# Performance work log

Measured on AMD Instinct MI355X. Metric: run time of the kernel, lower is better.

Reference implementation:

```python
import jax, jax.numpy as jnp
import numpy as np

B, T, D = 2, 2048, 2048
H, HKV, HD = 16, 8, 128
R = 128            # virtual memory tokens
DFF = 6144
MAX_ALPHA = 0.5
INFERENCE_SCALE = 1.0
EPS = 1e-6
NEG = -1e9


def _rms_norm(x, w):
    return x * jax.lax.rsqrt(jnp.mean(x * x, axis=-1, keepdims=True) + EPS) * w


def _rotate_half(x):
    x1, x2 = jnp.split(x, 2, axis=-1)
    return jnp.concatenate([-x2, x1], axis=-1)


def setup_inputs() -> dict:
    key = jax.random.key(0)
    ks = jax.random.split(key, 16)
    s = 0.02  # weight init scale
    hidden_states = jax.random.normal(ks[0], (B, T, D), jnp.float32)
    key_extra = jax.random.normal(ks[1], (B, HKV, R, HD), jnp.float32)
    value_extra = jax.random.normal(ks[2], (B, HKV, R, HD), jnp.float32)
    # RoPE tables (rope_theta = 1e6 as in Qwen3)
    inv_freq = 1.0 / (1e6 ** (jnp.arange(0, HD, 2, dtype=jnp.float32) / HD))
    freqs = jnp.arange(T, dtype=jnp.float32)[:, None] * inv_freq[None, :]  # (T, HD/2)
    emb = jnp.concatenate([freqs, freqs], axis=-1)  # (T, HD)
    cos, sin = jnp.cos(emb), jnp.sin(emb)
    # additive causal mask (B,1,T,T)
    causal = jnp.tril(jnp.ones((T, T), dtype=bool))
    attention_mask = jnp.where(causal, 0.0, NEG).astype(jnp.float32)
    attention_mask = jnp.broadcast_to(attention_mask[None, None], (B, 1, T, T))
    init_alpha, max_alpha = 0.1, MAX_ALPHA
    alpha_logit = jnp.float32(np.log(init_alpha / (max_alpha - init_alpha + 1e-8)))
    return {
        "hidden_states": hidden_states,
        "key_extra": key_extra,
        "value_extra": value_extra,
        "cos": cos,
        "sin": sin,
        "attention_mask": attention_mask,
        "alpha_logit": alpha_logit,
        "Wq": jax.random.normal(ks[3], (D, H * HD), jnp.float32) * s,
        "Wk": jax.random.normal(ks[4], (D, HKV * HD), jnp.float32) * s,
        "Wv": jax.random.normal(ks[5], (D, HKV * HD), jnp.float32) * s,
        "Wo": jax.random.normal(ks[6], (H * HD, D), jnp.float32) * s,
        "q_norm_w": jnp.ones((HD,), jnp.float32),
        "k_norm_w": jnp.ones((HD,), jnp.float32),
        "ln1_w": jnp.ones((D,), jnp.float32),
        "ln2_w": jnp.ones((D,), jnp.float32),
        "Wg": jax.random.normal(ks[7], (D, DFF), jnp.float32) * s,
        "Wu": jax.random.normal(ks[8], (D, DFF), jnp.float32) * s,
        "Wd": jax.random.normal(ks[9], (DFF, D), jnp.float32) * s,
    }


def reference(hidden_states, key_extra, value_extra, cos, sin, attention_mask,
              alpha_logit, Wq, Wk, Wv, Wo, q_norm_w, k_norm_w, ln1_w, ln2_w,
              Wg, Wu, Wd):
    Bq, Tq, Dq = hidden_states.shape
    G = H // HKV  # num_key_value_groups
    scaling = HD ** -0.5

    # ---- alpha scaling of raw memory KV (RawKVInjector.get_alpha) ----
    alpha = MAX_ALPHA * jax.nn.sigmoid(alpha_logit)
    eff = alpha * INFERENCE_SCALE
    k_extra = key_extra * eff
    v_extra = value_extra * eff

    # ---- decoder layer: input_layernorm ----
    residual = hidden_states
    h = _rms_norm(hidden_states, ln1_w)

    # ---- QKV projections + per-head RMSNorm ----
    q = _rms_norm((h @ Wq).reshape(Bq, Tq, H, HD), q_norm_w).transpose(0, 2, 1, 3)    # (B,H,T,hd)
    k = _rms_norm((h @ Wk).reshape(Bq, Tq, HKV, HD), k_norm_w).transpose(0, 2, 1, 3)  # (B,Hkv,T,hd)
    v = (h @ Wv).reshape(Bq, Tq, HKV, HD).transpose(0, 2, 1, 3)                        # (B,Hkv,T,hd)

    # ---- RoPE (applied before virtual-KV concat; virtual tokens get no RoPE) ----
    c, s_ = cos[None, None], sin[None, None]  # (1,1,T,hd)
    q = q * c + _rotate_half(q) * s_
    k = k * c + _rotate_half(k) * s_

    # ---- prepend virtual memory KV ----
    k_all = jnp.concatenate([k_extra, k], axis=2)  # (B,Hkv,R+T,hd)
    v_all = jnp.concatenate([v_extra, v], axis=2)
    Tk = R + Tq

    # mask: virtual tokens fully visible (zeros), then causal
    virtual_mask = jnp.zeros((Bq, 1, Tq, R), attention_mask.dtype)
    mask_full = jnp.concatenate([virtual_mask, attention_mask], axis=-1)  # (B,1,T,R+T)

    # ---- GQA attention (grouped einsum == repeat_kv + matmul) ----
    qg = q.reshape(Bq, HKV, G, Tq, HD)
    scores = jnp.einsum('bkgth,bksh->bkgts', qg, k_all) * scaling  # (B,Hkv,G,T,Tk)
    scores = scores + mask_full[:, :, None]
    probs = jax.nn.softmax(scores.astype(jnp.float32), axis=-1).astype(q.dtype)
    attn = jnp.einsum('bkgts,bksh->bkgth', probs, v_all)           # (B,Hkv,G,T,hd)
    attn = attn.reshape(Bq, H, Tq, HD).transpose(0, 2, 1, 3).reshape(Bq, Tq, H * HD)
    attn = attn @ Wo

    hidden = residual + attn

    # ---- MLP (SwiGLU) ----
    residual = hidden
    h2 = _rms_norm(hidden, ln2_w)
    mlp = (jax.nn.silu(h2 @ Wg) * (h2 @ Wu)) @ Wd
    return residual + mlp
```

## Files before the change

kernel.cpp:

```cpp
#include <hip/hip_runtime.h>
#include <hip/hip_bf16.h>


#define DEV __device__ __forceinline__

using f32x4  = __attribute__((ext_vector_type(4))) float;
using bf16x8 = __attribute__((ext_vector_type(8))) short;

constexpr int B_ = 2, T_ = 2048, D_ = 2048, H_ = 16, HKV_ = 8, HD_ = 128;
constexpr int R_ = 128, DFF_ = 6144, TK_ = R_ + T_;
constexpr int NT64_ = TK_ / 64;
constexpr int QKVW_ = 4096;
constexpr float EPS_ = 1e-6f;
constexpr float SCALING_ = 0.08838834764831845f;

DEV float bf2f(unsigned short u) {
  unsigned int x = ((unsigned int)u) << 16;
  return __builtin_bit_cast(float, x);
}
DEV unsigned short f2bf(float f) {
  unsigned int x = __builtin_bit_cast(unsigned int, f);
  x += 0x7fffu + ((x >> 16) & 1u);
  return (unsigned short)(x >> 16);
}

DEV void gload_lds16(const void* g, void* l) {
  __builtin_amdgcn_global_load_lds((__attribute__((address_space(1))) void*)(g),
                                   (__attribute__((address_space(3))) void*)(l),
                                   16, 0, 0);
}

__global__ __launch_bounds__(256) void k_rmsnorm(const float* __restrict__ x,
                                                 const float* __restrict__ w,
                                                 unsigned short* __restrict__ out) {
  const int row = blockIdx.x;
  const float* xr = x + (size_t)row * D_;
  const int t8 = threadIdx.x * 8;
  float4 a = *(const float4*)(xr + t8);
  float4 b = *(const float4*)(xr + t8 + 4);
  float ss = a.x*a.x + a.y*a.y + a.z*a.z + a.w*a.w
           + b.x*b.x + b.y*b.y + b.z*b.z + b.w*b.w;
  #pragma unroll
  for (int m = 1; m < 64; m <<= 1) ss += __shfl_xor(ss, m);
  __shared__ float red[4];
  if ((threadIdx.x & 63) == 0) red[threadIdx.x >> 6] = ss;
  __syncthreads();
  ss = red[0] + red[1] + red[2] + red[3];
  const float sc = rsqrtf(ss * (1.0f / D_) + EPS_);
  float4 wa = *(const float4*)(w + t8);
  float4 wb = *(const float4*)(w + t8 + 4);
  bf16x8 ov;
  ov[0] = (short)f2bf(a.x * sc * wa.x); ov[1] = (short)f2bf(a.y * sc * wa.y);
  ov[2] = (short)f2bf(a.z * sc * wa.z); ov[3] = (short)f2bf(a.w * sc * wa.w);
  ov[4] = (short)f2bf(b.x * sc * wb.x); ov[5] = (short)f2bf(b.y * sc * wb.y);
  ov[6] = (short)f2bf(b.z * sc * wb.z); ov[7] = (short)f2bf(b.w * sc * wb.w);
  *(bf16x8*)(out + (size_t)row * D_ + t8) = ov;
}

__global__ __launch_bounds__(256) void k_rms2(const float* __restrict__ p0,
                                              const float* __restrict__ p1,
                                              const float* __restrict__ hs,
                                              const float* __restrict__ w,
                                              float* __restrict__ hidden,
                                              unsigned short* __restrict__ out) {
  const int row = blockIdx.x;
  const size_t base = (size_t)row * D_ + threadIdx.x * 8;
  float4 a0 = *(const float4*)(p0 + base), a1 = *(const float4*)(p0 + base + 4);
  float4 b0 = *(const float4*)(p1 + base), b1 = *(const float4*)(p1 + base + 4);
  float4 c0 = *(const float4*)(hs + base), c1 = *(const float4*)(hs + base + 4);
  float4 va, vb;
  va.x = a0.x + b0.x + c0.x; va.y = a0.y + b0.y + c0.y;
  va.z = a0.z + b0.z + c0.z; va.w = a0.w + b0.w + c0.w;
  vb.x = a1.x + b1.x + c1.x; vb.y = a1.y + b1.y + c1.y;
  vb.z = a1.z + b1.z + c1.z; vb.w = a1.w + b1.w + c1.w;
  *(float4*)(hidden + base) = va;
  *(float4*)(hidden + base + 4) = vb;
  float ss = va.x*va.x + va.y*va.y + va.z*va.z + va.w*va.w
           + vb.x*vb.x + vb.y*vb.y + vb.z*vb.z + vb.w*vb.w;
  #pragma unroll
  for (int m = 1; m < 64; m <<= 1) ss += __shfl_xor(ss, m);
  __shared__ float red[4];
  if ((threadIdx.x & 63) == 0) red[threadIdx.x >> 6] = ss;
  __syncthreads();
  ss = red[0] + red[1] + red[2] + red[3];
  const float sc = rsqrtf(ss * (1.0f / D_) + EPS_);
  const int t8 = threadIdx.x * 8;
  float4 wa = *(const float4*)(w + t8);
  float4 wb = *(const float4*)(w + t8 + 4);
  bf16x8 ov;
  ov[0] = (short)f2bf(va.x * sc * wa.x); ov[1] = (short)f2bf(va.y * sc * wa.y);
  ov[2] = (short)f2bf(va.z * sc * wa.z); ov[3] = (short)f2bf(va.w * sc * wa.w);
  ov[4] = (short)f2bf(vb.x * sc * wb.x); ov[5] = (short)f2bf(vb.y * sc * wb.y);
  ov[6] = (short)f2bf(vb.z * sc * wb.z); ov[7] = (short)f2bf(vb.w * sc * wb.w);
  *(bf16x8*)(out + (size_t)row * D_ + t8) = ov;
}

__global__ __launch_bounds__(256) void k_finaladd(const float* __restrict__ p0,
                                                  const float* __restrict__ p1,
                                                  const float* __restrict__ hidden,
                                                  float* __restrict__ out) {
  const size_t i = ((size_t)blockIdx.x * 256 + threadIdx.x) * 4;
  float4 a = *(const float4*)(p0 + i);
  float4 b = *(const float4*)(p1 + i);
  float4 c = *(const float4*)(hidden + i);
  float4 o;
  o.x = a.x + b.x + c.x; o.y = a.y + b.y + c.y;
  o.z = a.z + b.z + c.z; o.w = a.w + b.w + c.w;
  *(float4*)(out + i) = o;
}

__global__ __launch_bounds__(256) void k_wtrans(const float* __restrict__ W,
                                                unsigned short* __restrict__ Wt,
                                                int K, int N) {
  __shared__ float tile[32][33];
  const int n0 = blockIdx.x * 32, k0 = blockIdx.y * 32;
  {
    const int kl = threadIdx.x >> 3, nc = (threadIdx.x & 7) * 4;
    float4 f = *(const float4*)(W + (size_t)(k0 + kl) * N + n0 + nc);
    tile[kl][nc] = f.x; tile[kl][nc + 1] = f.y;
    tile[kl][nc + 2] = f.z; tile[kl][nc + 3] = f.w;
  }
  __syncthreads();
  const int nl = threadIdx.x >> 3, kc = (threadIdx.x & 7) * 4;
  ushort4 o;
  o.x = f2bf(tile[kc][nl]);     o.y = f2bf(tile[kc + 1][nl]);
  o.z = f2bf(tile[kc + 2][nl]); o.w = f2bf(tile[kc + 3][nl]);
  *(ushort4*)(Wt + (size_t)(n0 + nl) * K + k0 + kc) = o;
}

template <int EPI>
__global__ __launch_bounds__(512, 2) void k_gemm(const unsigned short* __restrict__ A,
                                                 const unsigned short* __restrict__ Bt,
                                                 void* __restrict__ Cp,
                                                 const unsigned short* __restrict__ gmul,
                                                 int M, int ldc, int K) {
  __shared__ __align__(16) char lds[4 * 32768];
  const int tid = threadIdx.x, lane = tid & 63, wave = tid >> 6;
  const int wm = wave >> 2, wn = wave & 3;

  const int nbx = (int)gridDim.x;
  const int nwg = nbx * (int)gridDim.y;
  int bid = (int)blockIdx.y * nbx + (int)blockIdx.x;
  bid = (bid & 7) * (nwg >> 3) + (bid >> 3);
  const int glen = 4 * nbx;
  const int gid = bid / glen, rem = bid - gid * glen;
  const int row0 = (gid * 4 + (rem & 3)) * 256;
  const int col0 = (rem >> 2) * 256;

  const int kz = (int)blockIdx.z;
  const int Klocal = K / (int)gridDim.z;
  const int kbeg = kz * Klocal;
  const int NK = Klocal / 32;

  const int srow = wave * 16 + (lane >> 2);
  const int selem = (((lane & 3) ^ ((lane >> 3) & 3)) << 3);
  const unsigned short* pa = A  + (size_t)(row0 + srow) * K + kbeg + selem;
  const unsigned short* pb = Bt + (size_t)(col0 + srow) * K + kbeg + selem;
  const size_t rstep = (size_t)128 * K;
  char* const l = (char*)lds;
  const int woff = wave * 1024;

  f32x4 acc[8][4];
  #pragma unroll
  for (int i = 0; i < 8; i++)
    #pragma unroll
    for (int j = 0; j < 4; j++) acc[i][j] = {0.f, 0.f, 0.f, 0.f};

  auto STAGE = [&](int t) {
    char* s = l + (t & 3) * 32768;
    const unsigned short* a = pa + (size_t)t * 32;
    const unsigned short* b = pb + (size_t)t * 32;
    gload_lds16(a,         s + woff);
    gload_lds16(a + rstep, s + 8192 + woff);
    gload_lds16(b,         s + 16384 + woff);
    gload_lds16(b + rstep, s + 24576 + woff);
  };

  STAGE(0); STAGE(1); STAGE(2);

  const int rdcb = (((lane >> 4) ^ ((lane >> 1) & 3)) << 4);
  const int arow0 = wm * 128 + (lane & 15);
  const int brow0 = wn * 64 + (lane & 15);

#define TILE(VM, TT, DOSTAGE)                                                  \
  {                                                                            \
    asm volatile("s_waitcnt vmcnt(" #VM ")" ::: "memory");                     \
    __builtin_amdgcn_sched_barrier(0);                                         \
    __builtin_amdgcn_s_barrier();                                              \
    __builtin_amdgcn_sched_barrier(0);                                         \
    if (DOSTAGE) STAGE((TT) + 3);                                              \
    const char* sa = l + ((TT) & 3) * 32768;                                   \
    const char* sb = sa + 16384;                                               \
    bf16x8 af[8], bfr[4];                                                      \
    _Pragma("unroll")                                                          \
    for (int mi = 0; mi < 8; mi++)                                             \
      af[mi] = *(const bf16x8*)(sa + (arow0 + mi * 16) * 64 + rdcb);           \
    _Pragma("unroll")                                                          \
    for (int ni = 0; ni < 4; ni++)                                             \
      bfr[ni] = *(const bf16x8*)(sb + (brow0 + ni * 16) * 64 + rdcb);          \
    __builtin_amdgcn_s_setprio(1);                                             \
    _Pragma("unroll")                                                          \
    for (int mi = 0; mi < 8; mi++)                                             \
      _Pragma("unroll")                                                        \
      for (int ni = 0; ni < 4; ni++)                                           \
        acc[mi][ni] = __builtin_amdgcn_mfma_f32_16x16x32_bf16(af[mi], bfr[ni], \
                                                              acc[mi][ni], 0, 0, 0); \
    __builtin_amdgcn_s_setprio(0);                                             \
  }

  for (int t = 0; t < NK - 3; ++t) TILE(8, t, true)
  TILE(8, NK - 3, false)
  TILE(4, NK - 2, false)
  TILE(0, NK - 1, false)
#undef TILE

  const int crow = row0 + wm * 128 + ((lane >> 4) * 4);
  const int ccol = col0 + wn * 64 + (lane & 15);
  #pragma unroll
  for (int mi = 0; mi < 8; mi++)
    #pragma unroll
    for (int ni = 0; ni < 4; ni++) {
      const int r = crow + mi * 16;
      const int c = ccol + ni * 16;
      if constexpr (EPI == 0) {
        unsigned short* C = (unsigned short*)Cp;
        #pragma unroll
        for (int j = 0; j < 4; j++) C[(size_t)(r + j) * ldc + c] = f2bf(acc[mi][ni][j]);
      } else if constexpr (EPI == 2) {
        unsigned short* C = (unsigned short*)Cp;
        #pragma unroll
        for (int j = 0; j < 4; j++) {
          const float gx = bf2f(gmul[(size_t)(r + j) * ldc + c]);
          C[(size_t)(r + j) * ldc + c] = f2bf(gx / (1.f + __expf(-gx)) * acc[mi][ni][j]);
        }
      } else {
        float* C = (float*)Cp + (size_t)kz * M * ldc;
        #pragma unroll
        for (int j = 0; j < 4; j++) C[(size_t)(r + j) * ldc + c] = acc[mi][ni][j];
      }
    }
}

template <int ISQ>
__global__ __launch_bounds__(256) void k_qknorm(const unsigned short* __restrict__ qkv,
                                                const float* __restrict__ nw,
                                                const float* __restrict__ cosT,
                                                const float* __restrict__ sinT,
                                                unsigned short* __restrict__ out) {
  const int NH = ISQ ? H_ : HKV_;
  const int HOFF = ISQ ? 0 : H_;
  const int r = blockIdx.x * 16 + (threadIdx.x >> 4);
  const int l16 = threadIdx.x & 15;
  const int hd0 = l16 * 8;
  const int b = r / (T_ * NH), rem = r % (T_ * NH);
  const int t = rem / NH, hh = rem % NH;
  bf16x8 v = *(const bf16x8*)(qkv + (size_t)(b * T_ + t) * QKVW_ + (HOFF + hh) * HD_ + hd0);
  float f[8];
  float ss = 0.f;
  #pragma unroll
  for (int j = 0; j < 8; j++) { f[j] = bf2f((unsigned short)v[j]); ss += f[j] * f[j]; }
  #pragma unroll
  for (int m = 1; m < 16; m <<= 1) ss += __shfl_xor(ss, m);
  const float sc = rsqrtf(ss * (1.0f / HD_) + EPS_);
  float4 wa = *(const float4*)(nw + hd0);
  float4 wb = *(const float4*)(nw + hd0 + 4);
  float nv[8];
  nv[0] = f[0] * sc * wa.x; nv[1] = f[1] * sc * wa.y;
  nv[2] = f[2] * sc * wa.z; nv[3] = f[3] * sc * wa.w;
  nv[4] = f[4] * sc * wb.x; nv[5] = f[5] * sc * wb.y;
  nv[6] = f[6] * sc * wb.z; nv[7] = f[7] * sc * wb.w;
  const float sgn = (hd0 < 64) ? -1.f : 1.f;
  float rot[8];
  #pragma unroll
  for (int j = 0; j < 8; j++) rot[j] = sgn * __shfl_xor(nv[j], 8);
  const float* cr = cosT + (size_t)t * HD_ + hd0;
  const float* sr = sinT + (size_t)t * HD_ + hd0;
  float4 ca = *(const float4*)cr, cb = *(const float4*)(cr + 4);
  float4 sa = *(const float4*)sr, sb = *(const float4*)(sr + 4);
  const float cv[8] = {ca.x, ca.y, ca.z, ca.w, cb.x, cb.y, cb.z, cb.w};
  const float sv[8] = {sa.x, sa.y, sa.z, sa.w, sb.x, sb.y, sb.z, sb.w};
  bf16x8 ov;
  #pragma unroll
  for (int j = 0; j < 8; j++) ov[j] = (short)f2bf(nv[j] * cv[j] + rot[j] * sv[j]);
  if (ISQ) *(bf16x8*)(out + (((size_t)b * H_ + hh) * T_ + t) * HD_ + hd0) = ov;
  else     *(bf16x8*)(out + (((size_t)b * HKV_ + hh) * TK_ + R_ + t) * HD_ + hd0) = ov;
}

__global__ __launch_bounds__(256) void k_kvirt(const float* __restrict__ ke,
                                               const float* __restrict__ alog,
                                               unsigned short* __restrict__ k_all) {
  const size_t i = (size_t)blockIdx.x * 256 + threadIdx.x;
  const float eff = 0.5f / (1.f + __expf(-alog[0]));
  const int hd = (int)(i & 127);
  const int r  = (int)((i >> 7) & 127);
  const int bk = (int)(i >> 14);
  k_all[((size_t)bk * TK_ + r) * HD_ + hd] = f2bf(ke[i] * eff);
}

__global__ __launch_bounds__(256) void k_vbuild(const unsigned short* __restrict__ qkv,
                                                const float* __restrict__ ve,
                                                const float* __restrict__ alog,
                                                unsigned short* __restrict__ vT) {
  __shared__ float tile[32][33];
  const int kt = blockIdx.x, ht = blockIdx.y, bk = blockIdx.z;
  const int b = bk >> 3, kvh = bk & 7;
  const float eff = 0.5f / (1.f + __expf(-alog[0]));
  const int kl = threadIdx.x >> 3, hc = (threadIdx.x & 7) * 4;
  const int key = kt * 32 + kl, hd0 = ht * 32;
  if (key < R_) {
    float4 f = *(const float4*)(ve + (((size_t)(b * HKV_ + kvh) * R_ + key) * HD_ + hd0 + hc));
    tile[kl][hc] = f.x * eff; tile[kl][hc + 1] = f.y * eff;
    tile[kl][hc + 2] = f.z * eff; tile[kl][hc + 3] = f.w * eff;
  } else {
    const unsigned short* s = qkv + (size_t)(b * T_ + key - R_) * QKVW_
                              + (H_ + HKV_ + kvh) * HD_ + hd0 + hc;
    ushort4 u = *(const ushort4*)s;
    tile[kl][hc] = bf2f(u.x); tile[kl][hc + 1] = bf2f(u.y);
    tile[kl][hc + 2] = bf2f(u.z); tile[kl][hc + 3] = bf2f(u.w);
  }
  __syncthreads();
  const int hl = threadIdx.x >> 3, kc = (threadIdx.x & 7) * 4;
  ushort4 o;
  o.x = f2bf(tile[kc][hl]);     o.y = f2bf(tile[kc + 1][hl]);
  o.z = f2bf(tile[kc + 2][hl]); o.w = f2bf(tile[kc + 3][hl]);
  const int c0 = (kt & 1) * 32 + kc;
  const int p0 = ((c0 >> 5) << 5) | (((c0 >> 2) & 3) << 3) | (((c0 >> 4) & 1) << 2);
  *(ushort4*)(vT + ((size_t)bk * NT64_ + (kt >> 1)) * (HD_ * 64)
                  + (size_t)(hd0 + hl) * 64 + p0) = o;
}

__global__ __launch_bounds__(256, 2) void k_attn(const unsigned short* __restrict__ qr,
                                                 const unsigned short* __restrict__ k_all,
                                                 const unsigned short* __restrict__ vT,
                                                 unsigned short* __restrict__ out) {
  __shared__ __align__(16) unsigned short kT[2][64 * 128];
  __shared__ __align__(16) unsigned short vS[2][128 * 64];
  const int tid = threadIdx.x, lane = tid & 63, w = tid >> 6;
  const int qb = (int)gridDim.x - 1 - (int)blockIdx.x;
  const int h = blockIdx.y, b = blockIdx.z;
  const int kvh = h >> 1;
  const int q0 = qb * 128;

  bf16x8 qf[2][4];
  #pragma unroll
  for (int fq = 0; fq < 2; fq++) {
    const unsigned short* qbase =
        qr + ((size_t)((b * H_ + h) * T_) + q0 + w * 32 + fq * 16 + (lane & 15)) * HD_ + (lane >> 4) * 8;
    #pragma unroll
    for (int kc = 0; kc < 4; kc++) qf[fq][kc] = *(const bf16x8*)(qbase + kc * 32);
  }

  f32x4 zero = {0.f, 0.f, 0.f, 0.f};
  f32x4 o[2][8];
  #pragma unroll
  for (int fq = 0; fq < 2; fq++)
    #pragma unroll
    for (int i = 0; i < 8; i++) o[fq][i] = zero;
  float mrow[2] = {-3e38f, -3e38f}, lrow[2] = {0.f, 0.f};

  const int kr0 = w * 4 + (lane >> 4);
  const char* kSrc = (const char*)(k_all + (size_t)(b * HKV_ + kvh) * TK_ * HD_)
                     + (size_t)kr0 * 256 + (((lane & 15) * 16) ^ ((kr0 & 7) << 4));
  const char* vSrc = (const char*)(vT + (size_t)(b * HKV_ + kvh) * NT64_ * HD_ * 64)
                     + (size_t)(w * 8 + (lane >> 3)) * 128
                     + (((lane & 7) * 16) ^ (((lane >> 3) & 7) << 4));
  char* kL = (char*)kT;
  char* vL = (char*)vS;
  const int ldsw = w * 1024;

  const int ntiles = 2 * qb + 4;
  #pragma unroll
  for (int i = 0; i < 4; i++) {
    gload_lds16(kSrc + i * 4096, kL + ldsw + i * 4096);
    gload_lds16(vSrc + i * 4096, vL + ldsw + i * 4096);
  }
  int cur = 0;

  for (int it = 0; it < ntiles; ++it) {
    __syncthreads();
    if (it + 1 < ntiles) {
      const char* ks = kSrc + (size_t)(it + 1) * 16384;
      const char* vs = vSrc + (size_t)(it + 1) * 16384;
      char* kd = kL + ((cur ^ 1) * 16384 + ldsw);
      char* vd = vL + ((cur ^ 1) * 16384 + ldsw);
      #pragma unroll
      for (int i = 0; i < 4; i++) {
        gload_lds16(ks + i * 4096, kd + i * 4096);
        gload_lds16(vs + i * 4096, vd + i * 4096);
      }
    }
    const char* kTc = kL + cur * 16384;
    const char* vSc = vL + cur * 16384;

    f32x4 s[2][4];
    #pragma unroll
    for (int ni = 0; ni < 4; ni++) { s[0][ni] = zero; s[1][ni] = zero; }
    #pragma unroll
    for (int ni = 0; ni < 4; ni++) {
      const int rk = ni * 16 + (lane & 15);
      const int swz = (rk & 7) << 4;
      #pragma unroll
      for (int kc = 0; kc < 4; kc++) {
        bf16x8 kf = *(const bf16x8*)(kTc + ((rk * 256 + kc * 64 + (lane >> 4) * 16) ^ swz));
        s[0][ni] = __builtin_amdgcn_mfma_f32_16x16x32_bf16(kf, qf[0][kc], s[0][ni], 0, 0, 0);
        s[1][ni] = __builtin_amdgcn_mfma_f32_16x16x32_bf16(kf, qf[1][kc], s[1][ni], 0, 0, 0);
      }
    }

    const bool domask = (it >= ntiles - 2);
    bf16x8 pa[2][2];
    #pragma unroll
    for (int fq = 0; fq < 2; fq++) {
      const int q = q0 + w * 32 + fq * 16 + (lane & 15);
      #pragma unroll
      for (int ni = 0; ni < 4; ni++)
        #pragma unroll
        for (int j = 0; j < 4; j++) {
          float v = s[fq][ni][j] * SCALING_;
          if (domask) {
            const int key = it * 64 + ni * 16 + (lane >> 4) * 4 + j;
            if (key > R_ + q) v = -3e38f;
          }
          s[fq][ni][j] = v;
        }
      float pm = -3e38f;
      #pragma unroll
      for (int ni = 0; ni < 4; ni++)
        #pragma unroll
        for (int j = 0; j < 4; j++) pm = fmaxf(pm, s[fq][ni][j]);
      pm = fmaxf(pm, __shfl_xor(pm, 16));
      pm = fmaxf(pm, __shfl_xor(pm, 32));
      const float mn = fmaxf(mrow[fq], pm);
      const float scl = __expf(mrow[fq] - mn);
      mrow[fq] = mn;
      float rs = 0.f;
      #pragma unroll
      for (int ni = 0; ni < 4; ni++)
        #pragma unroll
        for (int j = 0; j < 4; j++) {
          const float p = __expf(s[fq][ni][j] - mn);
          s[fq][ni][j] = p;
          rs += p;
        }
      rs += __shfl_xor(rs, 16);
      rs += __shfl_xor(rs, 32);
      lrow[fq] = lrow[fq] * scl + rs;
      #pragma unroll
      for (int kc2 = 0; kc2 < 2; kc2++) {
        bf16x8 t;
        #pragma unroll
        for (int j = 0; j < 4; j++) {
          t[j]     = (short)f2bf(s[fq][2 * kc2][j]);
          t[4 + j] = (short)f2bf(s[fq][2 * kc2 + 1][j]);
        }
        pa[fq][kc2] = t;
      }
      #pragma unroll
      for (int j = 0; j < 4; j++) {
        const float sj = __shfl(scl, (lane & 48) | (((lane >> 4) << 2) + j));
        #pragma unroll
        for (int ni = 0; ni < 8; ni++) o[fq][ni][j] *= sj;
      }
    }

    #pragma unroll
    for (int kc2 = 0; kc2 < 2; kc2++) {
      #pragma unroll
      for (int ni = 0; ni < 8; ni++) {
        const int rv = ni * 16 + (lane & 15);
        bf16x8 vb = *(const bf16x8*)(vSc + ((rv * 128 + kc2 * 64 + (lane >> 4) * 16) ^ ((rv & 7) << 4)));
        o[0][ni] = __builtin_amdgcn_mfma_f32_16x16x32_bf16(pa[0][kc2], vb, o[0][ni], 0, 0, 0);
        o[1][ni] = __builtin_amdgcn_mfma_f32_16x16x32_bf16(pa[1][kc2], vb, o[1][ni], 0, 0, 0);
      }
    }
    cur ^= 1;
  }

  #pragma unroll
  for (int fq = 0; fq < 2; fq++) {
    float linv[4];
    #pragma unroll
    for (int j = 0; j < 4; j++)
      linv[j] = 1.f / __shfl(lrow[fq], (lane & 48) | (((lane >> 4) << 2) + j));
    const size_t orow = ((size_t)b * T_ + q0 + w * 32 + fq * 16 + (lane >> 4) * 4) * (H_ * HD_)
                        + h * HD_ + (lane & 15);
    #pragma unroll
    for (int ni = 0; ni < 8; ni++)
      #pragma unroll
      for (int j = 0; j < 4; j++)
        out[orow + (size_t)j * (H_ * HD_) + ni * 16] = f2bf(o[fq][ni][j] * linv[j]);
  }
}

extern "C" void kernel_launch(void* const* d_in, const int* in_sizes, int n_in,
                              void* d_out, int out_size, void* d_ws, size_t ws_size,
                              hipStream_t stream) {
  const float* hs   = (const float*)d_in[0];
  const float* ke   = (const float*)d_in[1];
  const float* ve   = (const float*)d_in[2];
  const float* cosT = (const float*)d_in[3];
  const float* sinT = (const float*)d_in[4];
  const float* alog = (const float*)d_in[6];
  const float* Wq   = (const float*)d_in[7];
  const float* Wk   = (const float*)d_in[8];
  const float* Wv   = (const float*)d_in[9];
  const float* Wo   = (const float*)d_in[10];
  const float* qnw  = (const float*)d_in[11];
  const float* knw  = (const float*)d_in[12];
  const float* ln1  = (const float*)d_in[13];
  const float* ln2  = (const float*)d_in[14];
  const float* Wg   = (const float*)d_in[15];
  const float* Wu   = (const float*)d_in[16];
  const float* Wd   = (const float*)d_in[17];

  char* ws = (char*)d_ws;
  size_t off = 0;
  auto alloc = [&](size_t bytes) {
    void* p = ws + off;
    off += (bytes + 255) & ~(size_t)255;
    return p;
  };
  const int M = B_ * T_;
  unsigned short* h     = (unsigned short*)alloc((size_t)M * D_ * 2);
  unsigned short* wt    = (unsigned short*)alloc((size_t)DFF_ * D_ * 2);
  unsigned short* qkv   = (unsigned short*)alloc((size_t)M * QKVW_ * 2);
  unsigned short* qrope = (unsigned short*)alloc((size_t)B_ * H_ * T_ * HD_ * 2);
  unsigned short* kall  = (unsigned short*)alloc((size_t)B_ * HKV_ * TK_ * HD_ * 2);
  unsigned short* vallT = (unsigned short*)alloc((size_t)B_ * HKV_ * (size_t)NT64_ * HD_ * 64 * 2);
  unsigned short* attno = (unsigned short*)alloc((size_t)M * 2048 * 2);
  float*          hidden= (float*)alloc((size_t)M * D_ * 4);
  unsigned short* g     = (unsigned short*)alloc((size_t)M * DFF_ * 2);
  float* part = (float*)qkv;

  k_rmsnorm<<<M, 256, 0, stream>>>(hs, ln1, h);
  k_wtrans<<<dim3(2048 / 32, 2048 / 32), 256, 0, stream>>>(Wq, wt, 2048, 2048);
  k_wtrans<<<dim3(1024 / 32, 2048 / 32), 256, 0, stream>>>(Wk, wt + (size_t)2048 * 2048, 2048, 1024);
  k_wtrans<<<dim3(1024 / 32, 2048 / 32), 256, 0, stream>>>(Wv, wt + (size_t)3072 * 2048, 2048, 1024);
  k_gemm<0><<<dim3(QKVW_ / 256, M / 256), 512, 0, stream>>>(h, wt, qkv, nullptr, M, QKVW_, 2048);
  k_qknorm<1><<<(B_ * T_ * H_) / 16, 256, 0, stream>>>(qkv, qnw, cosT, sinT, qrope);
  k_qknorm<0><<<(B_ * T_ * HKV_) / 16, 256, 0, stream>>>(qkv, knw, cosT, sinT, kall);
  k_kvirt<<<(B_ * HKV_ * R_ * HD_) / 256, 256, 0, stream>>>(ke, alog, kall);
  k_vbuild<<<dim3(TK_ / 32, HD_ / 32, B_ * HKV_), 256, 0, stream>>>(qkv, ve, alog, vallT);
  k_attn<<<dim3(T_ / 128, H_, B_), 256, 0, stream>>>(qrope, kall, vallT, attno);
  k_wtrans<<<dim3(2048 / 32, 2048 / 32), 256, 0, stream>>>(Wo, wt, 2048, 2048);
  k_gemm<3><<<dim3(2048 / 256, M / 256, 2), 512, 0, stream>>>(attno, wt, part, nullptr, M, 2048, 2048);
  k_rms2<<<M, 256, 0, stream>>>(part, part + (size_t)M * 2048, hs, ln2, hidden, h);
  k_wtrans<<<dim3(DFF_ / 32, 2048 / 32), 256, 0, stream>>>(Wg, wt, 2048, DFF_);
  k_gemm<0><<<dim3(DFF_ / 256, M / 256), 512, 0, stream>>>(h, wt, g, nullptr, M, DFF_, 2048);
  k_wtrans<<<dim3(DFF_ / 32, 2048 / 32), 256, 0, stream>>>(Wu, wt, 2048, DFF_);
  k_gemm<2><<<dim3(DFF_ / 256, M / 256), 512, 0, stream>>>(h, wt, g, g, M, DFF_, 2048);
  k_wtrans<<<dim3(2048 / 32, DFF_ / 32), 256, 0, stream>>>(Wd, wt, DFF_, 2048);
  k_gemm<3><<<dim3(2048 / 256, M / 256, 2), 512, 0, stream>>>(g, wt, part, nullptr, M, 2048, DFF_);
  k_finaladd<<<(M * 2048 / 4) / 256, 256, 0, stream>>>(part, part + (size_t)M * 2048, hidden, (float*)d_out);
}
```

Before: 705.4 us.

## Split GEMM k-step into two half-M phases with separate A/B staging

Restructures the GEMM main loop so each 32-wide k step runs as two phases, each covering half the M fragments, with A and B tile loads issued separately between them and extra barriers around each phase. Fewer A fragments are held in registers at once, and launch bounds drop to one block per CU. The aim is to interleave global-to-LDS loads with MFMA work more finely and to relieve register pressure. In exchange it doubles the barrier count and halves occupancy, which can expose latency.

```diff
diff --git a/kernel.cpp b/kernel.cpp
--- a/kernel.cpp
+++ b/kernel.cpp
@@ -129,7 +129,7 @@
 }
 
 template <int EPI>
-__global__ __launch_bounds__(512, 2) void k_gemm(const unsigned short* __restrict__ A,
+__global__ __launch_bounds__(512, 1) void k_gemm(const unsigned short* __restrict__ A,
                                                  const unsigned short* __restrict__ Bt,
                                                  void* __restrict__ Cp,
                                                  const unsigned short* __restrict__ gmul,
@@ -150,7 +150,7 @@
   const int kz = (int)blockIdx.z;
   const int Klocal = K / (int)gridDim.z;
   const int kbeg = kz * Klocal;
-  const int NK = Klocal / 32;
+  const int NKH = Klocal / 32;
 
   const int srow = wave * 16 + (lane >> 2);
   const int selem = (((lane & 3) ^ ((lane >> 3) & 3)) << 3);
@@ -166,53 +166,92 @@
     #pragma unroll
     for (int j = 0; j < 4; j++) acc[i][j] = {0.f, 0.f, 0.f, 0.f};
 
-  auto STAGE = [&](int t) {
-    char* s = l + (t & 3) * 32768;
-    const unsigned short* a = pa + (size_t)t * 32;
-    const unsigned short* b = pb + (size_t)t * 32;
+  auto STAGE_A = [&](int kh) {
+    char* s = l + (kh & 3) * 32768;
+    const unsigned short* a = pa + (size_t)kh * 32;
     gload_lds16(a,         s + woff);
     gload_lds16(a + rstep, s + 8192 + woff);
-    gload_lds16(b,         s + 16384 + woff);
-    gload_lds16(b + rstep, s + 24576 + woff);
   };
-
-  STAGE(0); STAGE(1); STAGE(2);
+  auto STAGE_B = [&](int kh) {
+    char* s = l + (kh & 3) * 32768 + 16384;
+    const unsigned short* b = pb + (size_t)kh * 32;
+    gload_lds16(b,         s + woff);
+    gload_lds16(b + rstep, s + 8192 + woff);
+  };
+
+  STAGE_A(0); STAGE_B(0); STAGE_A(1); STAGE_B(1); STAGE_A(2); STAGE_B(2);
+  asm volatile("s_waitcnt vmcnt(8)" ::: "memory");
+  __builtin_amdgcn_sched_barrier(0);
+  __builtin_amdgcn_s_barrier();
 
   const int rdcb = (((lane >> 4) ^ ((lane >> 1) & 3)) << 4);
   const int arow0 = wm * 128 + (lane & 15);
   const int brow0 = wn * 64 + (lane & 15);
-
-#define TILE(VM, TT, DOSTAGE)                                                  \
+  bf16x8 bfr[4];
+
+#define VMW(N) \
+    asm volatile("s_waitcnt vmcnt(" #N ")" ::: "memory");                      \
+    __builtin_amdgcn_sched_barrier(0);
+
+#define PHASE_A(KH, DOSTAGE)                                                   \
   {                                                                            \
-    asm volatile("s_waitcnt vmcnt(" #VM ")" ::: "memory");                     \
-    __builtin_amdgcn_sched_barrier(0);                                         \
-    __builtin_amdgcn_s_barrier();                                              \
-    __builtin_amdgcn_sched_barrier(0);                                         \
-    if (DOSTAGE) STAGE((TT) + 3);                                              \
-    const char* sa = l + ((TT) & 3) * 32768;                                   \
+    const char* sa = l + ((KH) & 3) * 32768;                                   \
     const char* sb = sa + 16384;                                               \
-    bf16x8 af[8], bfr[4];                                                      \
+    bf16x8 af[4];                                                              \
     _Pragma("unroll")                                                          \
-    for (int mi = 0; mi < 8; mi++)                                             \
+    for (int mi = 0; mi < 4; mi++)                                             \
       af[mi] = *(const bf16x8*)(sa + (arow0 + mi * 16) * 64 + rdcb);           \
     _Pragma("unroll")                                                          \
     for (int ni = 0; ni < 4; ni++)                                             \
       bfr[ni] = *(const bf16x8*)(sb + (brow0 + ni * 16) * 64 + rdcb);          \
+    if (DOSTAGE) STAGE_A((KH) + 3);                                            \
+    __builtin_amdgcn_s_barrier();                                              \
+    asm volatile("s_waitcnt lgkmcnt(0)" ::: "memory");                         \
+    __builtin_amdgcn_sched_barrier(0);                                         \
     __builtin_amdgcn_s_setprio(1);                                             \
     _Pragma("unroll")                                                          \
-    for (int mi = 0; mi < 8; mi++)                                             \
+    for (int mi = 0; mi < 4; mi++)                                             \
       _Pragma("unroll")                                                        \
       for (int ni = 0; ni < 4; ni++)                                           \
         acc[mi][ni] = __builtin_amdgcn_mfma_f32_16x16x32_bf16(af[mi], bfr[ni], \
                                                               acc[mi][ni], 0, 0, 0); \
     __builtin_amdgcn_s_setprio(0);                                             \
-  }
-
-  for (int t = 0; t < NK - 3; ++t) TILE(8, t, true)
-  TILE(8, NK - 3, false)
-  TILE(4, NK - 2, false)
-  TILE(0, NK - 1, false)
-#undef TILE
+    __builtin_amdgcn_s_barrier();                                              \
+  }
+
+#define PHASE_B(KH, DOSTAGE, VMCODE)                                           \
+  {                                                                            \
+    const char* sa = l + ((KH) & 3) * 32768;                                   \
+    bf16x8 af[4];                                                              \
+    _Pragma("unroll")                                                          \
+    for (int mi = 0; mi < 4; mi++)                                             \
+      af[mi] = *(const bf16x8*)(sa + (arow0 + (mi + 4) * 16) * 64 + rdcb);     \
+    if (DOSTAGE) STAGE_B((KH) + 3);                                            \
+    __builtin_amdgcn_s_barrier();                                              \
+    asm volatile("s_waitcnt lgkmcnt(0)" ::: "memory");                         \
+    __builtin_amdgcn_sched_barrier(0);                                         \
+    __builtin_amdgcn_s_setprio(1);                                             \
+    _Pragma("unroll")                                                          \
+    for (int mi = 0; mi < 4; mi++)                                             \
+      _Pragma("unroll")                                                        \
+      for (int ni = 0; ni < 4; ni++)                                           \
+        acc[mi + 4][ni] = __builtin_amdgcn_mfma_f32_16x16x32_bf16(af[mi], bfr[ni], \
+                                                                  acc[mi + 4][ni], 0, 0, 0); \
+    __builtin_amdgcn_s_setprio(0);                                             \
+    VMCODE                                                                     \
+    __builtin_amdgcn_s_barrier();                                              \
+  }
+
+  for (int kh = 0; kh < NKH - 3; ++kh) {
+    PHASE_A(kh, true)
+    PHASE_B(kh, true, VMW(8))
+  }
+  PHASE_A(NKH - 3, false) PHASE_B(NKH - 3, false, VMW(4))
+  PHASE_A(NKH - 2, false) PHASE_B(NKH - 2, false, VMW(0))
+  PHASE_A(NKH - 1, false) PHASE_B(NKH - 1, false, )
+#undef PHASE_A
+#undef PHASE_B
+#undef VMW
 
   const int crow = row0 + wm * 128 + ((lane >> 4) * 4);
   const int ccol = col0 + wn * 64 + (lane & 15);
```

After: 704.0 us. Within noise of the previous version (-0.2%).

## Restructure GEMM main loop into 8-phase ping-pong schedule with finer-grained staging

Applied to the files above, without the earlier changes.

Reworks the bf16 MFMA GEMM mainloop from a 4-slot 32-wide K pipeline into a 2-buffer 64-wide K tile that is split into eight phases. Each phase reads part of the LDS fragments, issues one slice of the global-to-LDS prefetch, and runs half the MFMAs, with explicit barriers and vmcnt waits between phases. This interleaves loads and compute more finely to hide memory latency. The workgroup swizzle grouping also changes from 4 rows to 2 rows. The extra barriers per K step and the hand-tuned wait counts add sync overhead and correctness risk.

```diff
diff --git a/kernel.cpp b/kernel.cpp
--- a/kernel.cpp
+++ b/kernel.cpp
@@ -134,7 +134,7 @@
                                                  void* __restrict__ Cp,
                                                  const unsigned short* __restrict__ gmul,
                                                  int M, int ldc, int K) {
-  __shared__ __align__(16) char lds[4 * 32768];
+  __shared__ __align__(16) char lds[2 * 65536];
   const int tid = threadIdx.x, lane = tid & 63, wave = tid >> 6;
   const int wm = wave >> 2, wn = wave & 3;
 
@@ -142,15 +142,16 @@
   const int nwg = nbx * (int)gridDim.y;
   int bid = (int)blockIdx.y * nbx + (int)blockIdx.x;
   bid = (bid & 7) * (nwg >> 3) + (bid >> 3);
-  const int glen = 4 * nbx;
+  const int glen = 2 * nbx;
   const int gid = bid / glen, rem = bid - gid * glen;
-  const int row0 = (gid * 4 + (rem & 3)) * 256;
-  const int col0 = (rem >> 2) * 256;
+  const int row0 = (gid * 2 + (rem & 1)) * 256;
+  const int col0 = (rem >> 1) * 256;
 
   const int kz = (int)blockIdx.z;
   const int Klocal = K / (int)gridDim.z;
   const int kbeg = kz * Klocal;
-  const int NK = Klocal / 32;
+  const int NT = Klocal / 64;
+  const int NI = NT / 2;
 
   const int srow = wave * 16 + (lane >> 2);
   const int selem = (((lane & 3) ^ ((lane >> 3) & 3)) << 3);
@@ -166,53 +167,81 @@
     #pragma unroll
     for (int j = 0; j < 4; j++) acc[i][j] = {0.f, 0.f, 0.f, 0.f};
 
-  auto STAGE = [&](int t) {
-    char* s = l + (t & 3) * 32768;
-    const unsigned short* a = pa + (size_t)t * 32;
-    const unsigned short* b = pb + (size_t)t * 32;
-    gload_lds16(a,         s + woff);
-    gload_lds16(a + rstep, s + 8192 + woff);
-    gload_lds16(b,         s + 16384 + woff);
-    gload_lds16(b + rstep, s + 24576 + woff);
+  auto STAGE_H = [&](int hh) {
+    if (hh >= 4 * NT) return;
+    const int t = hh >> 2, p = hh & 3;
+    const unsigned short* src = ((p & 1) ? pb : pa) + (size_t)t * 64 + ((p >> 1) << 5);
+    char* dst = l + ((t & 1) << 16) + ((p & 1) << 15) + ((p >> 1) << 14) + woff;
+    gload_lds16(src, dst);
+    gload_lds16(src + rstep, dst + 8192);
   };
 
-  STAGE(0); STAGE(1); STAGE(2);
+  for (int hh = 0; hh < 8; ++hh) STAGE_H(hh);
+  asm volatile("s_waitcnt vmcnt(8)" ::: "memory");
+  __builtin_amdgcn_sched_barrier(0);
+  __builtin_amdgcn_s_barrier();
 
   const int rdcb = (((lane >> 4) ^ ((lane >> 1) & 3)) << 4);
   const int arow0 = wm * 128 + (lane & 15);
   const int brow0 = wn * 64 + (lane & 15);
 
-#define TILE(VM, TT, DOSTAGE)                                                  \
+  bf16x8 a[8], bfr[2];
+  int h = 8;
+
+#define MFMA_(x, y, z) __builtin_amdgcn_mfma_f32_16x16x32_bf16(x, y, z, 0, 0, 0)
+#define VMW(N) asm volatile("s_waitcnt vmcnt(" #N ")" ::: "memory"); \
+               __builtin_amdgcn_sched_barrier(0);
+
+#define PH(D, KK, NILO, READA, DOSTAGE, VMC)                                   \
   {                                                                            \
-    asm volatile("s_waitcnt vmcnt(" #VM ")" ::: "memory");                     \
+    if (READA) {                                                               \
+      _Pragma("unroll")                                                        \
+      for (int mi = 0; mi < 8; mi++)                                           \
+        a[mi] = *(const bf16x8*)(l + ((D) << 16) + ((KK) << 14) +              \
+                                 (arow0 + mi * 16) * 64 + rdcb);               \
+    }                                                                          \
+    bfr[0] = *(const bf16x8*)(l + ((D) << 16) + 32768 + ((KK) << 14) +         \
+                              (brow0 + (NILO) * 16) * 64 + rdcb);              \
+    bfr[1] = *(const bf16x8*)(l + ((D) << 16) + 32768 + ((KK) << 14) +         \
+                              (brow0 + (NILO) * 16 + 16) * 64 + rdcb);         \
+    if (DOSTAGE) { STAGE_H(h); h++; }                                          \
+    __builtin_amdgcn_s_barrier();                                              \
+    asm volatile("s_waitcnt lgkmcnt(0)" ::: "memory");                         \
     __builtin_amdgcn_sched_barrier(0);                                         \
-    __builtin_amdgcn_s_barrier();                                              \
-    __builtin_amdgcn_sched_barrier(0);                                         \
-    if (DOSTAGE) STAGE((TT) + 3);                                              \
-    const char* sa = l + ((TT) & 3) * 32768;                                   \
-    const char* sb = sa + 16384;                                               \
-    bf16x8 af[8], bfr[4];                                                      \
-    _Pragma("unroll")                                                          \
-    for (int mi = 0; mi < 8; mi++)                                             \
-      af[mi] = *(const bf16x8*)(sa + (arow0 + mi * 16) * 64 + rdcb);           \
-    _Pragma("unroll")                                                          \
-    for (int ni = 0; ni < 4; ni++)                                             \
-      bfr[ni] = *(const bf16x8*)(sb + (brow0 + ni * 16) * 64 + rdcb);          \
     __builtin_amdgcn_s_setprio(1);                                             \
     _Pragma("unroll")                                                          \
-    for (int mi = 0; mi < 8; mi++)                                             \
-      _Pragma("unroll")                                                        \
-      for (int ni = 0; ni < 4; ni++)                                           \
-        acc[mi][ni] = __builtin_amdgcn_mfma_f32_16x16x32_bf16(af[mi], bfr[ni], \
-                                                              acc[mi][ni], 0, 0, 0); \
+    for (int mi = 0; mi < 8; mi++) {                                           \
+      acc[mi][(NILO)]     = MFMA_(a[mi], bfr[0], acc[mi][(NILO)]);             \
+      acc[mi][(NILO) + 1] = MFMA_(a[mi], bfr[1], acc[mi][(NILO) + 1]);         \
+    }                                                                          \
     __builtin_amdgcn_s_setprio(0);                                             \
-  }
-
-  for (int t = 0; t < NK - 3; ++t) TILE(8, t, true)
-  TILE(8, NK - 3, false)
-  TILE(4, NK - 2, false)
-  TILE(0, NK - 1, false)
-#undef TILE
+    VMC                                                                        \
+    __builtin_amdgcn_s_barrier();                                              \
+  }
+
+  for (int it = 0; it < NI - 1; ++it) {
+    PH(0, 0, 0, true,  (it > 0), )
+    PH(0, 0, 2, false, true, )
+    PH(0, 1, 0, true,  true, )
+    PH(0, 1, 2, false, true, VMW(10))
+    PH(1, 0, 0, true,  true, )
+    PH(1, 0, 2, false, true, )
+    PH(1, 1, 0, true,  true, VMW(10))
+    PH(1, 1, 2, false, true, VMW(6))
+  }
+  {
+    PH(0, 0, 0, true,  true, )
+    PH(0, 0, 2, false, true, )
+    PH(0, 1, 0, true,  true, )
+    PH(0, 1, 2, false, true, VMW(4))
+    PH(1, 0, 0, true,  true, )
+    PH(1, 0, 2, false, true, VMW(0))
+    PH(1, 1, 0, true,  true, )
+    PH(1, 1, 2, false, true, )
+  }
+#undef PH
+#undef VMW
+#undef MFMA_
 
   const int crow = row0 + wm * 128 + ((lane >> 4) * 4);
   const int ccol = col0 + wn * 64 + (lane & 15);
```

Result: slower. 738.4 us (+4.7%).
